# Kernel tuning notes

Measured on AMD Instinct MI355X. Metric: run time of the kernel, lower is better.

Reference implementation:

```python
import jax, jax.numpy as jnp
import numpy as np

VOCAB, EMB = 5000, 300
UNITS = [256, 512, 256]  # two return_sequences layers + final return-last layer
DENSE = 64


def lstm_layer(x, W, U, b, return_seq):
    """Keras-style LSTM with activation='relu', recurrent_activation='sigmoid'.
    x: [B,T,D]; W: [D,4u]; U: [u,4u]; b: [4u]. Gate order: i, f, c, o."""
    B = x.shape[0]
    u = U.shape[0]
    xg = jnp.einsum('btd,dg->btg', x, W) + b  # precompute input projections [B,T,4u]

    def step(carry, xg_t):
        h, c = carry
        g = xg_t + h @ U
        i, f, cc, o = jnp.split(g, 4, axis=-1)
        i = jax.nn.sigmoid(i)
        f = jax.nn.sigmoid(f)
        o = jax.nn.sigmoid(o)
        c = f * c + i * jax.nn.relu(cc)
        h = o * jax.nn.relu(c)
        return (h, c), h

    h0 = jnp.zeros((B, u), x.dtype)
    (hT, _), hs = jax.lax.scan(step, (h0, h0), jnp.swapaxes(xg, 0, 1))
    return jnp.swapaxes(hs, 0, 1) if return_seq else hT


def setup_inputs() -> dict:
    key = jax.random.key(0)
    ks = iter(jax.random.split(key, 16))
    s = 0.05  # small init keeps relu-LSTM numerically stable
    inp = {
        'tokens': jax.random.randint(next(ks), (128, 512), 0, VOCAB, dtype=jnp.int32),
        'emb': jax.random.normal(next(ks), (VOCAB, EMB), jnp.float32) * s,
    }
    d = EMB
    for li, u in enumerate(UNITS):
        inp[f'W{li}'] = jax.random.normal(next(ks), (d, 4 * u), jnp.float32) * s
        inp[f'U{li}'] = jax.random.normal(next(ks), (u, 4 * u), jnp.float32) * s
        inp[f'b{li}'] = jnp.zeros((4 * u,), jnp.float32)
        d = u
    inp['Wd'] = jax.random.normal(next(ks), (UNITS[-1], DENSE), jnp.float32) * s
    inp['bd'] = jnp.zeros((DENSE,), jnp.float32)
    inp['Wc'] = jax.random.normal(next(ks), (DENSE, 1), jnp.float32) * s
    inp['bc'] = jnp.zeros((1,), jnp.float32)
    return inp


def reference(tokens, emb, W0, U0, b0, W1, U1, b1, W2, U2, b2, Wd, bd, Wc, bc):
    x = emb[tokens]                                   # [B,T,300]
    x = lstm_layer(x, W0, U0, b0, return_seq=True)    # [B,T,256]
    x = lstm_layer(x, W1, U1, b1, return_seq=True)    # [B,T,512]
    x = lstm_layer(x, W2, U2, b2, return_seq=False)   # [B,256]
    x = jax.nn.relu(x @ Wd + bd)                      # [B,64]
    return jax.nn.sigmoid(x @ Wc + bc)                # [B,1]
```

## Files before the change

kernel.cpp:

```cpp
#include <hip/hip_runtime.h>
#include <cstdint>
#include <cstddef>

#define BATCH  128
#define SEQT   512
#define EMB_D  300
#define VOCABN 5000
#define KP0    320
#define NU0    256
#define NU1    512
#define NU2    256
#define NDENSE 64
#define RING   32
#define LIM    (1 << 19)

typedef unsigned short ushortT;
typedef unsigned long long ull;
typedef __attribute__((ext_vector_type(8))) short bf16x8;
typedef __attribute__((ext_vector_type(8))) unsigned short u16x8;
typedef __attribute__((ext_vector_type(4))) unsigned short u16x4;
typedef __attribute__((ext_vector_type(4))) float f32x4;

#define AGT __HIP_MEMORY_SCOPE_AGENT

static __device__ __forceinline__ unsigned short f2bf(float x) {
    union { float f; unsigned u; } v; v.f = x;
    const unsigned r = v.u + 0x7FFFu + ((v.u >> 16) & 1u);
    return (unsigned short)(r >> 16);
}
static __device__ __forceinline__ float bf2f(unsigned short b) {
    union { unsigned u; float f; } v; v.u = ((unsigned)b) << 16;
    return v.f;
}
static __device__ __forceinline__ float sigmoidf_(float x) {
    return 1.f / (1.f + __expf(-x));
}
static __device__ __forceinline__ unsigned ald(const unsigned* p) {
    return __hip_atomic_load((unsigned*)p, __ATOMIC_RELAXED, AGT);
}
static __device__ __forceinline__ void ast(unsigned* p, unsigned v) {
    __hip_atomic_store(p, v, __ATOMIC_RELAXED, AGT);
}
static __device__ __forceinline__ void ld16c(u16x8* d, const void* p) {
    asm volatile("global_load_dwordx4 %0, %1, off sc0 sc1"
                 : "=&v"(*d) : "v"(p) : "memory");
}
static __device__ __forceinline__ void ld8c(u16x4* d, const void* p) {
    asm volatile("global_load_dwordx2 %0, %1, off sc0 sc1"
                 : "=&v"(*d) : "v"(p) : "memory");
}
static __device__ __forceinline__ void st4c(void* p, unsigned v) {
    asm volatile("global_store_dword %0, %1, off sc0 sc1"
                 :: "v"(p), "v"(v) : "memory");
}
static __device__ __forceinline__ void wait0() {
    asm volatile("s_waitcnt vmcnt(0)" ::: "memory");
    __builtin_amdgcn_sched_barrier(0);
}
static __device__ __forceinline__ void wait2() {
    asm volatile("s_waitcnt vmcnt(2)" ::: "memory");
    __builtin_amdgcn_sched_barrier(0);
}

__global__ __launch_bounds__(256) void convert_WT(
    const float* __restrict__ W, ushortT* __restrict__ WbfT,
    int K, int NG, int KP, int total)
{
    for (int idx = blockIdx.x * 256 + threadIdx.x; idx < total; idx += gridDim.x * 256) {
        const int m = idx / KP, k = idx - m * KP;
        WbfT[idx] = (k < K) ? f2bf(W[(size_t)k * NG + m]) : (ushortT)0;
    }
}
__global__ __launch_bounds__(256) void convert_emb(
    const float* __restrict__ emb, ushortT* __restrict__ embbf)
{
    const int total = VOCABN * KP0;
    for (int idx = blockIdx.x * 256 + threadIdx.x; idx < total; idx += gridDim.x * 256) {
        const int v = idx / KP0, k = idx - v * KP0;
        embbf[idx] = (k < EMB_D) ? f2bf(emb[(size_t)v * EMB_D + k]) : (ushortT)0;
    }
}

__global__ __launch_bounds__(256) void gemm_xg0(
    const ushortT* __restrict__ embbf,
    const int*   __restrict__ tokens,
    const ushortT* __restrict__ W0T,
    const float* __restrict__ bias,
    ushortT* __restrict__ xg0)
{
    __shared__ ushortT Wl[128][32];
    __shared__ ushortT Xl[128][32];
    __shared__ int tokL[128];

    const int tid = threadIdx.x;
    const int t   = blockIdx.x;
    const int m0  = blockIdx.y * 128;
    const int wv  = tid >> 6;
    const int lane = tid & 63;
    const int lo  = lane & 15;
    const int hi  = lane >> 4;

    if (tid < 128) tokL[tid] = tokens[tid * SEQT + t];
    __syncthreads();

    f32x4 acc[2][8];
    #pragma unroll
    for (int s = 0; s < 2; ++s)
        #pragma unroll
        for (int n = 0; n < 8; ++n)
            acc[s][n] = f32x4{0.f, 0.f, 0.f, 0.f};

    for (int k0 = 0; k0 < KP0; k0 += 32) {
        #pragma unroll
        for (int it = 0; it < 2; ++it) {
            const int idx = tid + it * 256;
            const int row = idx >> 2, gq = idx & 3;
            const int gs  = gq ^ ((row >> 1) & 3);
            *(u16x8*)&Wl[row][gs * 8] =
                *(const u16x8*)(W0T + (size_t)(m0 + row) * KP0 + k0 + gq * 8);
            *(u16x8*)&Xl[row][gs * 8] =
                *(const u16x8*)(embbf + (size_t)tokL[row] * KP0 + k0 + gq * 8);
        }
        __syncthreads();

        bf16x8 bfr[8];
        #pragma unroll
        for (int n = 0; n < 8; ++n) {
            const int row = n * 16 + lo;
            bfr[n] = *(const bf16x8*)&Xl[row][(hi ^ ((row >> 1) & 3)) * 8];
        }
        #pragma unroll
        for (int s = 0; s < 2; ++s) {
            const int row = wv * 32 + s * 16 + lo;
            const bf16x8 a = *(const bf16x8*)&Wl[row][(hi ^ ((row >> 1) & 3)) * 8];
            #pragma unroll
            for (int n = 0; n < 8; ++n)
                acc[s][n] = __builtin_amdgcn_mfma_f32_16x16x32_bf16(a, bfr[n], acc[s][n], 0, 0, 0);
        }
        __syncthreads();
    }

    #pragma unroll
    for (int s = 0; s < 2; ++s)
        #pragma unroll
        for (int j = 0; j < 4; ++j) {
            const int m = m0 + wv * 32 + s * 16 + hi * 4 + j;
            const float bi = bias[m];
            #pragma unroll
            for (int n = 0; n < 8; ++n)
                xg0[(((size_t)t * 8 + n) * 1024 + m) * 16 + lo] = f2bf(acc[s][n][j] + bi);
        }
}

template<int U_, bool XATOMIC, int XTSH, int XPH>
__device__ void rec_role(
    int rid,
    const float* __restrict__ Umat,
    const ushortT* __restrict__ xgring, int xmask,
    ushortT* __restrict__ hring,
    unsigned* Fown,
    unsigned* Xown,
    unsigned* Xguard, int nGd,
    char* smem)
{
    constexpr int NGu = 4 * U_;
    constexpr int WPG = U_ / 64;
    constexpr int KT  = U_ / 32;
    constexpr int GR  = U_ / 8;
    constexpr int NLD = (16 * GR) / 256;

    ushortT* hstage = (ushortT*)smem;

    const int tid = threadIdx.x, w = tid >> 6, lane = tid & 63;
    const int lo = lane & 15, hi = lane >> 4;
    const int grp = rid & 7, wgj = rid >> 3;
    const int b0 = grp * 16, J = wgj * 64;
    const int jcol = J + w * 16 + lo;
    const size_t S = (size_t)128 * U_;

    bf16x8 bfr[4][KT];
    #pragma unroll
    for (int g = 0; g < 4; ++g)
        #pragma unroll
        for (int kt = 0; kt < KT; ++kt) {
            const float* up = Umat + (size_t)(kt * 32 + hi * 8) * NGu + g * U_ + jcol;
            bf16x8 v;
            #pragma unroll
            for (int i = 0; i < 8; ++i) v[i] = (short)f2bf(up[(size_t)i * NGu]);
            bfr[g][kt] = v;
        }

    float creg[4] = {0.f, 0.f, 0.f, 0.f};

    if (XATOMIC) {
        if (w == 0) {
            int guard = 0; bool ok;
            do {
                bool pred = true;
                if (lane < 4) {
                    const int mt = (lane * U_ + J) >> XTSH;
                    pred = ((int)ald(&Xown[(mt * XPH) * 16]) >= 1);
                }
                ok = __all(pred);
                if (!ok) __builtin_amdgcn_s_sleep(2);
            } while (!ok && ++guard < LIM);
        }
        __syncthreads();
    }
    u16x4 xnext[4];
    {
        const size_t xb = (size_t)grp * NGu;
        #pragma unroll
        for (int g = 0; g < 4; ++g) {
            const ushortT* ap = xgring + (xb + g * U_ + jcol) * 16 + hi * 4;
            if (XATOMIC) ld8c(&xnext[g], ap);
            else         xnext[g] = *(const u16x4*)ap;
        }
        if (XATOMIC) wait0();
    }

    for (int t = 0; t < SEQT; ++t) {
        if (w == 0) {
            int guard = 0; bool ok;
            do {
                bool pred = true;
                if (t > 0 && lane < WPG)
                    pred = ((int)ald(&Fown[(grp * WPG + lane) * 16]) >= t);
                if (XATOMIC && t + 1 < SEQT && lane < 4) {
                    const int mt = (lane * U_ + J) >> XTSH;
                    const int fi = mt * XPH + ((t + 1) & (XPH - 1));
                    pred = pred && ((int)ald(&Xown[fi * 16]) >= t + 2);
                }
                for (int i = lane; i < nGd; i += 64)
                    pred = pred && ((int)ald(&Xguard[i * 16]) >= t - (RING - 1));
                ok = __all(pred);
                if (!ok) __builtin_amdgcn_s_sleep(1);
            } while (!ok && ++guard < LIM);
        }
        __syncthreads();

        u16x4 xcur[4];
        #pragma unroll
        for (int g = 0; g < 4; ++g) xcur[g] = xnext[g];

        u16x8 hr[NLD];
        if (t > 0) {
            const ushortT* hsrc = hring + (size_t)((t - 1) & (RING - 1)) * S;
            #pragma unroll
            for (int q = 0; q < NLD; ++q) {
                const int i = tid + q * 256;
                const int row = i / GR, gi = i - row * GR;
                ld16c(&hr[q], hsrc + (size_t)(b0 + row) * U_ + gi * 8);
            }
            wait0();
            #pragma unroll
            for (int q = 0; q < NLD; ++q) {
                const int i = tid + q * 256;
                const int row = i / GR, gi = i - row * GR;
                *(u16x8*)&hstage[(row * GR + (gi ^ (row & 7))) * 8] = hr[q];
            }
        }
        if (t + 1 < SEQT) {
            const size_t xb = (size_t)(((t + 1) & xmask) * 8 + grp) * NGu;
            #pragma unroll
            for (int g = 0; g < 4; ++g) {
                const ushortT* ap = xgring + (xb + g * U_ + jcol) * 16 + hi * 4;
                if (XATOMIC) ld8c(&xnext[g], ap);
                else         xnext[g] = *(const u16x4*)ap;
            }
        }
        __syncthreads();

        f32x4 acc[4];
        #pragma unroll
        for (int g = 0; g < 4; ++g) acc[g] = f32x4{0.f, 0.f, 0.f, 0.f};
        if (t > 0) {
            #pragma unroll
            for (int kt = 0; kt < KT; ++kt) {
                const int gs = (kt * 4 + hi) ^ (lo & 7);
                const bf16x8 a = *(const bf16x8*)&hstage[(lo * GR + gs) * 8];
                #pragma unroll
                for (int g = 0; g < 4; ++g)
                    acc[g] = __builtin_amdgcn_mfma_f32_16x16x32_bf16(a, bfr[g][kt], acc[g], 0, 0, 0);
            }
        }

        ushortT* hwr = hring + (size_t)(t & (RING - 1)) * S;
        unsigned own[4], oth[4];
        #pragma unroll
        for (int r = 0; r < 4; ++r) {
            const float i_ = sigmoidf_(acc[0][r] + bf2f(xcur[0][r]));
            const float f_ = sigmoidf_(acc[1][r] + bf2f(xcur[1][r]));
            const float cc = fmaxf(acc[2][r] + bf2f(xcur[2][r]), 0.f);
            const float o_ = sigmoidf_(acc[3][r] + bf2f(xcur[3][r]));
            creg[r] = f_ * creg[r] + i_ * cc;
            own[r] = (unsigned)f2bf(o_ * fmaxf(creg[r], 0.f));
        }
        #pragma unroll
        for (int r = 0; r < 4; ++r)
            oth[r] = (unsigned)__shfl_xor((int)own[r], 1);
        {
            const int odd = lo & 1;
            const int rb = odd ? 2 : 0;
            const int je = jcol - odd;
            #pragma unroll
            for (int q = 0; q < 2; ++q) {
                const int r = rb + q;
                const unsigned pk = odd ? (oth[r] | (own[r] << 16))
                                        : (own[r] | (oth[r] << 16));
                st4c(&hwr[(size_t)(b0 + hi * 4 + r) * U_ + je], pk);
            }
        }
        wait0();
        __syncthreads();
        if (tid == 0)
            ast(&Fown[(grp * WPG + wgj) * 16], (unsigned)(t + 1));
    }
}

template<int MC, int NGATES, int KP, int P>
__device__ void worker_role(
    int mtile, int phase,
    const ushortT* __restrict__ WT,
    const float* __restrict__ bias,
    const ushortT* __restrict__ hring,
    ushortT* __restrict__ xgring,
    unsigned* Fup, int nUp,
    unsigned* Fguard, int nGd,
    unsigned* Xrel,
    char* smem)
{
    constexpr int GR2 = KP / 8;
    constexpr int NIT = KP / 32;
    constexpr int WR  = MC / 4;
    constexpr int MT  = WR / 16;
    ushortT* Wl = (ushortT*)smem;
    ushortT* Xl = (ushortT*)(smem + (size_t)MC * KP * 2);

    const int tid = threadIdx.x, w = tid >> 6, lane = tid & 63;
    const int lo = lane & 15, hi = lane >> 4;
    const int m0 = mtile * MC;
    const int row = tid >> 1, gq0 = (tid & 1) * 2;
    const int gs0 = gq0 ^ ((row >> 1) & 3);
    const int gs1 = (gq0 + 1) ^ ((row >> 1) & 3);

    for (int i = tid; i < MC * GR2; i += 256) {
        const int r_ = i / GR2, gi = i - r_ * GR2;
        const int gs = gi ^ (r_ & 7);
        *(u16x8*)&Wl[(r_ * GR2 + gs) * 8] =
            *(const u16x8*)(WT + (size_t)(m0 + r_) * KP + gi * 8);
    }
    float bv[MT][4];
    #pragma unroll
    for (int mt = 0; mt < MT; ++mt)
        #pragma unroll
        for (int j = 0; j < 4; ++j)
            bv[mt][j] = bias[m0 + w * WR + mt * 16 + hi * 4 + j];
    __syncthreads();

    for (int t = phase; t < SEQT; t += P) {
        if (w == 0) {
            int guard = 0; bool ok;
            do {
                bool pred = true;
                for (int i = lane; i < nUp; i += 64)
                    pred = pred && ((int)ald(&Fup[i * 16]) >= t + 1);
                for (int i = lane; i < nGd; i += 64)
                    pred = pred && ((int)ald(&Fguard[i * 16]) >= t - (RING - 1));
                ok = __all(pred);
                if (!ok) __builtin_amdgcn_s_sleep(32);
            } while (!ok && ++guard < LIM);
        }
        __syncthreads();

        const ushortT* hslab = hring + (size_t)(t & (RING - 1)) * 128 * KP;

        f32x4 acc[MT][8];
        #pragma unroll
        for (int mt = 0; mt < MT; ++mt)
            #pragma unroll
            for (int nn = 0; nn < 8; ++nn) acc[mt][nn] = f32x4{0.f, 0.f, 0.f, 0.f};

        u16x8 Ra0, Ra1, Rb0, Rb1;
        ld16c(&Ra0, hslab + (size_t)row * KP + gq0 * 8);
        ld16c(&Ra1, hslab + (size_t)row * KP + (gq0 + 1) * 8);
        #pragma unroll
        for (int it = 0; it < NIT; ++it) {
            const bool even = ((it & 1) == 0);
            if (it + 1 < NIT) {
                const ushortT* np = hslab + (size_t)row * KP + (it + 1) * 32;
                if (even) { ld16c(&Rb0, np + gq0 * 8); ld16c(&Rb1, np + (gq0 + 1) * 8); }
                else      { ld16c(&Ra0, np + gq0 * 8); ld16c(&Ra1, np + (gq0 + 1) * 8); }
                wait2();
            } else {
                wait0();
            }
            ushortT* Xc = Xl + (it & 1) * (128 * 32);
            *(u16x8*)&Xc[row * 32 + gs0 * 8] = even ? Ra0 : Rb0;
            *(u16x8*)&Xc[row * 32 + gs1 * 8] = even ? Ra1 : Rb1;
            __syncthreads();
            #pragma unroll
            for (int mt = 0; mt < MT; ++mt) {
                const int arow = w * WR + mt * 16 + lo;
                const int gsa = (it * 4 + hi) ^ (arow & 7);
                const bf16x8 a = *(const bf16x8*)&Wl[(arow * GR2 + gsa) * 8];
                #pragma unroll
                for (int nn = 0; nn < 8; ++nn) {
                    const int brow = nn * 16 + lo;
                    const bf16x8 b = *(const bf16x8*)&Xc[brow * 32 + (hi ^ ((brow >> 1) & 3)) * 8];
                    acc[mt][nn] = __builtin_amdgcn_mfma_f32_16x16x32_bf16(a, b, acc[mt][nn], 0, 0, 0);
                }
            }
            __syncthreads();
        }

        const size_t slab = (size_t)(t & (RING - 1)) * 8;
        #pragma unroll
        for (int mt = 0; mt < MT; ++mt) {
            #pragma unroll
            for (int nn = 0; nn < 8; ++nn) {
                const int b = nn * 16 + lo;
                unsigned own[4], oth[4];
                #pragma unroll
                for (int j = 0; j < 4; ++j)
                    own[j] = (unsigned)f2bf(acc[mt][nn][j] + bv[mt][j]);
                #pragma unroll
                for (int j = 0; j < 4; ++j)
                    oth[j] = (unsigned)__shfl_xor((int)own[j], 1);
                const int odd = lo & 1;
                const int jb = odd ? 2 : 0;
                const int be = (b & 15) - odd;
                #pragma unroll
                for (int q = 0; q < 2; ++q) {
                    const int j = jb + q;
                    const int m = m0 + w * WR + mt * 16 + hi * 4 + j;
                    const unsigned pk = odd ? (oth[j] | (own[j] << 16))
                                            : (own[j] | (oth[j] << 16));
                    st4c(&xgring[((slab + nn) * NGATES + m) * 16 + be], pk);
                }
            }
        }
        wait0();
        __syncthreads();
        if (tid == 0)
            ast(Xrel, (unsigned)(t + 1));
    }
}

struct MegaArgs {
    const float *U0, *U1, *U2;
    const ushortT *W1T, *W2T;
    const float *b1, *b2;
    const ushortT* xg0;
    ushortT *xg1, *xg2;
    ushortT *h0r, *h1r, *h2r;
    unsigned *F0, *F1, *F2, *X1, *X2;
};

__global__ __launch_bounds__(256, 1) void mega(MegaArgs A)
{
    extern __shared__ char smem[];
    const int bid = blockIdx.x;
    if (bid < 32) {
        rec_role<NU0, false, 1, 1>(bid, A.U0, A.xg0, 511, A.h0r, A.F0,
                                   nullptr, A.X1, 64, smem);
    } else if (bid < 96) {
        rec_role<NU1, true, 8, 8>(bid - 32, A.U1, A.xg1, RING - 1, A.h1r, A.F1,
                                  A.X1, A.X2, 32, smem);
    } else if (bid < 128) {
        rec_role<NU2, true, 7, 4>(bid - 96, A.U2, A.xg2, RING - 1, A.h2r, A.F2,
                                  A.X2, nullptr, 0, smem);
    } else if (bid < 192) {
        const int wid = bid - 128;
        const int mt = wid & 7, ph = wid >> 3;
        worker_role<256, 2048, 256, 8>(mt, ph, A.W1T, A.b1, A.h0r, A.xg1,
                                       A.F0, 32, A.F1, 64, A.X1 + (mt * 8 + ph) * 16, smem);
    } else {
        const int wid = bid - 192;
        const int mt = wid & 7, ph = wid >> 3;
        worker_role<128, 1024, 512, 4>(mt, ph, A.W2T, A.b2, A.h1r, A.xg2,
                                       A.F1, 64, A.F2, 32, A.X2 + (mt * 4 + ph) * 16, smem);
    }
}

__global__ __launch_bounds__(64) void head_kernel(
    const ushortT* __restrict__ h2,
    const float* __restrict__ Wd,
    const float* __restrict__ bd,
    const float* __restrict__ Wc,
    const float* __restrict__ bc,
    float* __restrict__ out)
{
    const int b = blockIdx.x;
    const int j = threadIdx.x;
    float a = bd[j];
    const ushortT* hrow = h2 + (size_t)b * NU2;
    #pragma unroll 4
    for (int k = 0; k < NU2; ++k)
        a += bf2f(hrow[k]) * Wd[(size_t)k * NDENSE + j];
    a = fmaxf(a, 0.f) * Wc[j];
    #pragma unroll
    for (int off = 32; off > 0; off >>= 1)
        a += __shfl_down(a, off);
    if (j == 0)
        out[b] = 1.f / (1.f + expf(-(a + bc[0])));
}

extern "C" void kernel_launch(void* const* d_in, const int* in_sizes, int n_in,
                              void* d_out, int out_size, void* d_ws, size_t ws_size,
                              hipStream_t stream)
{
    const int*   tokens = (const int*)  d_in[0];
    const float* emb    = (const float*)d_in[1];
    const float* W0     = (const float*)d_in[2];
    const float* Ur0    = (const float*)d_in[3];
    const float* b0v    = (const float*)d_in[4];
    const float* W1     = (const float*)d_in[5];
    const float* Ur1    = (const float*)d_in[6];
    const float* b1v    = (const float*)d_in[7];
    const float* W2     = (const float*)d_in[8];
    const float* Ur2    = (const float*)d_in[9];
    const float* b2v    = (const float*)d_in[10];
    const float* Wd     = (const float*)d_in[11];
    const float* bd     = (const float*)d_in[12];
    const float* Wc     = (const float*)d_in[13];
    const float* bc     = (const float*)d_in[14];
    float* out = (float*)d_out;

    char* p = (char*)d_ws;
    auto alloc = [&](size_t bytes) -> char* {
        char* q = p; p += (bytes + 255) & ~(size_t)255; return q;
    };
    ushortT* xg0   = (ushortT*)alloc((size_t)SEQT * 8 * 1024 * 16 * 2);
    ushortT* xg1   = (ushortT*)alloc((size_t)RING * 8 * 2048 * 16 * 2);
    ushortT* xg2   = (ushortT*)alloc((size_t)RING * 8 * 1024 * 16 * 2);
    ushortT* h0r   = (ushortT*)alloc((size_t)RING * 128 * NU0 * 2);
    ushortT* h1r   = (ushortT*)alloc((size_t)RING * 128 * NU1 * 2);
    ushortT* h2r   = (ushortT*)alloc((size_t)RING * 128 * NU2 * 2);
    ushortT* W0T   = (ushortT*)alloc((size_t)1024 * KP0 * 2);
    ushortT* W1T   = (ushortT*)alloc((size_t)2048 * NU0 * 2);
    ushortT* W2T   = (ushortT*)alloc((size_t)1024 * NU1 * 2);
    ushortT* embbf = (ushortT*)alloc((size_t)VOCABN * KP0 * 2);
    unsigned* flg  = (unsigned*)alloc(32768);

    unsigned* F0 = flg;
    unsigned* F1 = F0 + 32 * 16;
    unsigned* F2 = F1 + 64 * 16;
    unsigned* X1 = F2 + 32 * 16;
    unsigned* X2 = X1 + 64 * 16;

    hipMemsetAsync(flg, 0, 32768, stream);

    convert_WT<<<512, 256, 0, stream>>>(W0, W0T, EMB_D, 1024, KP0, 1024 * KP0);
    convert_WT<<<512, 256, 0, stream>>>(W1, W1T, NU0, 2048, NU0, 2048 * NU0);
    convert_WT<<<512, 256, 0, stream>>>(W2, W2T, NU1, 1024, NU1, 1024 * NU1);
    convert_emb<<<1024, 256, 0, stream>>>(emb, embbf);

    gemm_xg0<<<dim3(SEQT, 8), 256, 0, stream>>>(embbf, tokens, W0T, b0v, xg0);

    MegaArgs A;
    A.U0 = Ur0; A.U1 = Ur1; A.U2 = Ur2;
    A.W1T = W1T; A.W2T = W2T;
    A.b1 = b1v; A.b2 = b2v;
    A.xg0 = xg0; A.xg1 = xg1; A.xg2 = xg2;
    A.h0r = h0r; A.h1r = h1r; A.h2r = h2r;
    A.F0 = F0; A.F1 = F1; A.F2 = F2; A.X1 = X1; A.X2 = X2;

    void* args[] = {&A};
    hipLaunchCooperativeKernel((void*)mega, dim3(224), dim3(256), args, 147456, stream);

    head_kernel<<<BATCH, 64, 0, stream>>>(h2r + (size_t)31 * 128 * NU2,
                                          Wd, bd, Wc, bc, out);
}
```

Measured before the change: 2.461 ms.

## Replace block-level barriers with per-wavefront flags in recurrent LSTM roles

Each wavefront now polls its dependency flags itself and publishes its own per-wave completion flag, instead of wave 0 polling then a __syncthreads, and a block barrier before a single thread signals. Flag arrays grow fourfold (one entry per wave), and the worker roles check more flags. The next-step xg prefetch is issued before waiting on the h loads (partial vmcnt wait), and the downstream-ring guard check is done only every 8 steps with a lookahead margin. The intent is to cut barrier and polling latency on the serial per-timestep critical path, at the cost of more flag traffic and more lanes spinning.

New measurement: 2.735 ms. 1.11x slower.

```diff
diff --git a/kernel.cpp b/kernel.cpp
--- a/kernel.cpp
+++ b/kernel.cpp
@@ -61,6 +61,10 @@
     asm volatile("s_waitcnt vmcnt(2)" ::: "memory");
     __builtin_amdgcn_sched_barrier(0);
 }
+static __device__ __forceinline__ void wait4() {
+    asm volatile("s_waitcnt vmcnt(4)" ::: "memory");
+    __builtin_amdgcn_sched_barrier(0);
+}
 
 __global__ __launch_bounds__(256) void convert_WT(
     const float* __restrict__ W, ushortT* __restrict__ WbfT,
@@ -165,6 +169,7 @@
 {
     constexpr int NGu = 4 * U_;
     constexpr int WPG = U_ / 64;
+    constexpr int NWF = WPG * 4;
     constexpr int KT  = U_ / 32;
     constexpr int GR  = U_ / 8;
     constexpr int NLD = (16 * GR) / 256;
@@ -193,19 +198,16 @@
     float creg[4] = {0.f, 0.f, 0.f, 0.f};
 
     if (XATOMIC) {
-        if (w == 0) {
-            int guard = 0; bool ok;
-            do {
-                bool pred = true;
-                if (lane < 4) {
-                    const int mt = (lane * U_ + J) >> XTSH;
-                    pred = ((int)ald(&Xown[(mt * XPH) * 16]) >= 1);
-                }
-                ok = __all(pred);
-                if (!ok) __builtin_amdgcn_s_sleep(2);
-            } while (!ok && ++guard < LIM);
-        }
-        __syncthreads();
+        int guard = 0; bool ok;
+        do {
+            bool pred = true;
+            if (lane < 4) {
+                const int mt = (lane * U_ + J) >> XTSH;
+                pred = ((int)ald(&Xown[(mt * XPH) * 16]) >= 1);
+            }
+            ok = __all(pred);
+            if (!ok) __builtin_amdgcn_s_sleep(2);
+        } while (!ok && ++guard < LIM);
     }
     u16x4 xnext[4];
     {
@@ -220,28 +222,29 @@
     }
 
     for (int t = 0; t < SEQT; ++t) {
-        if (w == 0) {
+        u16x4 xcur[4];
+        #pragma unroll
+        for (int g = 0; g < 4; ++g) xcur[g] = xnext[g];
+
+        {
             int guard = 0; bool ok;
             do {
                 bool pred = true;
-                if (t > 0 && lane < WPG)
-                    pred = ((int)ald(&Fown[(grp * WPG + lane) * 16]) >= t);
-                if (XATOMIC && t + 1 < SEQT && lane < 4) {
-                    const int mt = (lane * U_ + J) >> XTSH;
+                if (t > 0 && lane < NWF)
+                    pred = ((int)ald(&Fown[(grp * NWF + lane) * 16]) >= t);
+                if (XATOMIC && t + 1 < SEQT && lane >= 40 && lane < 44) {
+                    const int mt = ((lane - 40) * U_ + J) >> XTSH;
                     const int fi = mt * XPH + ((t + 1) & (XPH - 1));
                     pred = pred && ((int)ald(&Xown[fi * 16]) >= t + 2);
                 }
-                for (int i = lane; i < nGd; i += 64)
-                    pred = pred && ((int)ald(&Xguard[i * 16]) >= t - (RING - 1));
+                if (nGd && (t & 7) == 0) {
+                    for (int i = lane; i < nGd; i += 64)
+                        pred = pred && ((int)ald(&Xguard[i * 16]) >= t + 8 - (RING - 1));
+                }
                 ok = __all(pred);
                 if (!ok) __builtin_amdgcn_s_sleep(1);
             } while (!ok && ++guard < LIM);
         }
-        __syncthreads();
-
-        u16x4 xcur[4];
-        #pragma unroll
-        for (int g = 0; g < 4; ++g) xcur[g] = xnext[g];
 
         u16x8 hr[NLD];
         if (t > 0) {
@@ -252,21 +255,25 @@
                 const int row = i / GR, gi = i - row * GR;
                 ld16c(&hr[q], hsrc + (size_t)(b0 + row) * U_ + gi * 8);
             }
-            wait0();
+        }
+        const bool pf = (t + 1 < SEQT);
+        if (pf) {
+            const size_t xb = (size_t)(((t + 1) & xmask) * 8 + grp) * NGu;
+            #pragma unroll
+            for (int g = 0; g < 4; ++g) {
+                const ushortT* ap = xgring + (xb + g * U_ + jcol) * 16 + hi * 4;
+                if (XATOMIC) ld8c(&xnext[g], ap);
+                else         xnext[g] = *(const u16x4*)ap;
+            }
+        }
+        if (t > 0) {
+            if (XATOMIC && pf) wait4();
+            else               wait0();
             #pragma unroll
             for (int q = 0; q < NLD; ++q) {
                 const int i = tid + q * 256;
                 const int row = i / GR, gi = i - row * GR;
                 *(u16x8*)&hstage[(row * GR + (gi ^ (row & 7))) * 8] = hr[q];
-            }
-        }
-        if (t + 1 < SEQT) {
-            const size_t xb = (size_t)(((t + 1) & xmask) * 8 + grp) * NGu;
-            #pragma unroll
-            for (int g = 0; g < 4; ++g) {
-                const ushortT* ap = xgring + (xb + g * U_ + jcol) * 16 + hi * 4;
-                if (XATOMIC) ld8c(&xnext[g], ap);
-                else         xnext[g] = *(const u16x4*)ap;
             }
         }
         __syncthreads();
@@ -312,9 +319,8 @@
             }
         }
         wait0();
-        __syncthreads();
-        if (tid == 0)
-            ast(&Fown[(grp * WPG + wgj) * 16], (unsigned)(t + 1));
+        if (lane == 0)
+            ast(&Fown[(grp * NWF + wgj * 4 + w) * 16], (unsigned)(t + 1));
     }
 }
 
@@ -474,12 +480,12 @@
         const int wid = bid - 128;
         const int mt = wid & 7, ph = wid >> 3;
         worker_role<256, 2048, 256, 8>(mt, ph, A.W1T, A.b1, A.h0r, A.xg1,
-                                       A.F0, 32, A.F1, 64, A.X1 + (mt * 8 + ph) * 16, smem);
+                                       A.F0, 128, A.F1, 256, A.X1 + (mt * 8 + ph) * 16, smem);
     } else {
         const int wid = bid - 192;
         const int mt = wid & 7, ph = wid >> 3;
         worker_role<128, 1024, 512, 4>(mt, ph, A.W2T, A.b2, A.h1r, A.xg2,
-                                       A.F1, 64, A.F2, 32, A.X2 + (mt * 4 + ph) * 16, smem);
+                                       A.F1, 256, A.F2, 128, A.X2 + (mt * 4 + ph) * 16, smem);
     }
 }
 
@@ -541,15 +547,15 @@
     ushortT* W1T   = (ushortT*)alloc((size_t)2048 * NU0 * 2);
     ushortT* W2T   = (ushortT*)alloc((size_t)1024 * NU1 * 2);
     ushortT* embbf = (ushortT*)alloc((size_t)VOCABN * KP0 * 2);
-    unsigned* flg  = (unsigned*)alloc(32768);
+    unsigned* flg  = (unsigned*)alloc(65536);
 
     unsigned* F0 = flg;
-    unsigned* F1 = F0 + 32 * 16;
-    unsigned* F2 = F1 + 64 * 16;
-    unsigned* X1 = F2 + 32 * 16;
+    unsigned* F1 = F0 + 128 * 16;
+    unsigned* F2 = F1 + 256 * 16;
+    unsigned* X1 = F2 + 128 * 16;
     unsigned* X2 = X1 + 64 * 16;
 
-    hipMemsetAsync(flg, 0, 32768, stream);
+    hipMemsetAsync(flg, 0, 65536, stream);
 
     convert_WT<<<512, 256, 0, stream>>>(W0, W0T, EMB_D, 1024, KP0, 1024 * KP0);
     convert_WT<<<512, 256, 0, stream>>>(W1, W1T, NU0, 2048, NU0, 2048 * NU0);
```
